# Performance work log

Hardware: AMD Instinct MI355X
Metric: run time of the kernel (lower is better)

Reference implementation:

```python
import jax, jax.numpy as jnp
import numpy as np

B, D, T = 16, 512, 2048
H = 2
HD = D // H

def setup_inputs() -> dict:
    key = jax.random.key(0)
    k1, k2, k3, k4 = jax.random.split(key, 4)
    s_in = 1.0 / np.sqrt(D)   # torch default-like uniform init for weight_matrix
    s_t = 1.0 / np.sqrt(T)    # nn.Linear default init bound
    xs = jax.random.normal(k1, (B, D, T), dtype=jnp.float32)
    W_KQ = jax.random.uniform(k2, (D, D), jnp.float32, -s_in, s_in)
    W_PV = jax.random.uniform(k3, (D, D), jnp.float32, -s_in, s_in)
    W_out = jax.random.uniform(k4, (T, T), jnp.float32, -s_t, s_t)
    return {"xs": xs, "W_KQ": W_KQ, "W_PV": W_PV, "W_out": W_out}

def reference(xs, W_KQ, W_PV, W_out):
    b, d, t = xs.shape
    xs_skip = xs[:, :, :-1]                                   # [B, D, T-1]
    # xskq = xs_skip^T @ W_KQ  -> [B, T-1, D]
    xskq = jnp.einsum('bds,dj->bsj', xs_skip, W_KQ)
    # split heads: [B, H, T-1, HD]
    xskq_split = xskq.reshape(b, t - 1, H, HD).transpose(0, 2, 1, 3)
    # xs reshaped to heads along feature dim: [B, H, HD, T]
    xs_r = xs.reshape(b, H, HD, t)
    attn_arg = jnp.matmul(xskq_split, xs_r)                   # [B, H, T-1, T], rho=1
    # NON-STANDARD: softmax over the head axis (size 2)
    sm = jax.nn.softmax(attn_arg, axis=1)
    # W_PV @ xs_skip -> [B, D, T-1], split into heads [B, H, HD, T-1]
    wpvx = jnp.einsum('id,bds->bis', W_PV, xs_skip).reshape(b, H, HD, t - 1)
    f_attn = jnp.matmul(wpvx, sm).reshape(b, d, t)            # [B, D, T]
    # output = Linear(T, T, bias=None) then take last token:
    # out[b, i] = sum_t f_attn[b, i, t] * W_out[T-1, t]
    out = jnp.einsum('bdt,t->bd', f_attn, W_out[-1])
    return out
```

## Files before the change

kernel.cpp:

```cpp
#include <hip/hip_runtime.h>
#include <hip/hip_bf16.h>

#define NB 16
#define ND 512
#define NT 2048
#define TM1 2047
#define NHD 256

typedef __attribute__((ext_vector_type(8))) short bf16x8;
typedef __attribute__((ext_vector_type(4))) float f32x4;
typedef unsigned short ushort_t;
typedef unsigned int uint_t;

#define G0_OFF    0ull
#define R0_OFF    32768ull
#define SX_OFF    40960ull
#define WSUM_OFF  49152ull
#define WKQT_OFF  49408ull
#define CHUNK_OFF 180480ull
#define BATCH_US  (2048ull * 512ull)
#define BATCH_FLOATS (2ull * 524288ull)

__device__ __forceinline__ ushort_t f2bf(float x) {
    union { float f; uint_t u; } v; v.f = x;
    uint_t r = v.u + 0x7FFFu + ((v.u >> 16) & 1u);
    return (ushort_t)(r >> 16);
}
__device__ __forceinline__ float bf2f(uint_t u) {
    union { uint_t u; float f; } v; v.u = u << 16;
    return v.f;
}

__device__ __forceinline__ void async_copy16(const ushort_t* g, ushort_t* l) {
    __builtin_amdgcn_global_load_lds(
        (const __attribute__((address_space(1))) void*)g,
        (__attribute__((address_space(3))) void*)l, 16, 0, 0);
}

#define FENCE() asm volatile("" ::: "memory")
#define BARRIER() do { FENCE(); __builtin_amdgcn_s_barrier(); FENCE(); } while (0)
#define WAITVM4() asm volatile("s_waitcnt vmcnt(4)" ::: "memory")
#define WAITVM0() asm volatile("s_waitcnt vmcnt(0)" ::: "memory")

__global__ __launch_bounds__(256) void k_cvt_xst(const float* __restrict__ xs,
                                                 ushort_t* __restrict__ xst, int b0,
                                                 const float* __restrict__ wkq,
                                                 ushort_t* __restrict__ wkqT,
                                                 const float* __restrict__ wlast,
                                                 float* __restrict__ wsum,
                                                 float* __restrict__ sxacc) {
    __shared__ float tile[64][257];
    __shared__ float sxl[64];
    const int t0 = blockIdx.x * 256, d0 = blockIdx.y * 64;
    const int cc = blockIdx.z;
    const float* xb = xs + (size_t)(b0 + cc) * ND * NT;
    ushort_t* xo = xst + (size_t)cc * BATCH_US;
    const int wave = threadIdx.x >> 6, lane = threadIdx.x & 63;
    if (threadIdx.x < 64) sxl[threadIdx.x] = 0.f;
    #pragma unroll
    for (int i = 0; i < 16; ++i) {
        const int row = wave * 16 + i;
        *(float4*)&tile[row][lane * 4] =
            *(const float4*)&xb[(size_t)(d0 + row) * NT + t0 + lane * 4];
    }
    __syncthreads();
    const int c8 = (threadIdx.x & 7) * 8;
    float sxp[8] = {0.f, 0.f, 0.f, 0.f, 0.f, 0.f, 0.f, 0.f};
    #pragma unroll
    for (int i = 0; i < 8; ++i) {
        const int t = i * 32 + (threadIdx.x >> 3);
        uint_t w[4];
        #pragma unroll
        for (int p = 0; p < 4; ++p)
            w[p] = (uint_t)f2bf(tile[c8 + 2 * p][t]) |
                   ((uint_t)f2bf(tile[c8 + 2 * p + 1][t]) << 16);
        *(uint4*)&xo[(size_t)(t0 + t) * ND + d0 + c8] = *(uint4*)w;
        if (t0 + t != 2047) {
            #pragma unroll
            for (int p = 0; p < 8; ++p) sxp[p] += tile[c8 + p][t];
        }
    }
    #pragma unroll
    for (int p = 0; p < 8; ++p) atomicAdd(&sxl[c8 + p], sxp[p]);
    __syncthreads();
    if (threadIdx.x < 64)
        atomicAdd(&sxacc[(size_t)(b0 + cc) * ND + d0 + threadIdx.x], sxl[threadIdx.x]);
    if (cc == 0 && b0 == 0) {
        __shared__ float ptile[32][33];
        const int bid = blockIdx.y * 8 + blockIdx.x;
        const int c = threadIdx.x & 31, r = threadIdx.x >> 5;
        #pragma unroll 1
        for (int q = 0; q < 4; ++q) {
            const int job = bid * 4 + q;
            const int j0 = (job & 15) * 32, dd0 = (job >> 4) * 32;
            __syncthreads();
            #pragma unroll
            for (int i = 0; i < 4; ++i)
                ptile[r + i * 8][c] = wkq[(size_t)(dd0 + r + i * 8) * ND + j0 + c];
            __syncthreads();
            #pragma unroll
            for (int i = 0; i < 4; ++i)
                wkqT[(size_t)(j0 + r + i * 8) * ND + dd0 + c] = f2bf(ptile[c][r + i * 8]);
        }
        if (bid == 0) {
            __shared__ float red[256];
            float s = 0.f;
            for (int t = threadIdx.x; t < NT; t += 256) s += wlast[t];
            red[threadIdx.x] = s;
            __syncthreads();
            for (int off = 128; off > 0; off >>= 1) {
                if (threadIdx.x < off) red[threadIdx.x] += red[threadIdx.x + off];
                __syncthreads();
            }
            if (threadIdx.x == 0) *wsum = red[0];
        }
    }
}

__device__ __forceinline__ void ld_frag4(bf16x8 (&dst)[4][2], const ushort_t* buf,
                                         int rbase, int l15, int quad, int swz) {
    #pragma unroll
    for (int i = 0; i < 4; ++i)
        #pragma unroll
        for (int kc = 0; kc < 2; ++kc)
            dst[i][kc] = *(const bf16x8*)&buf[(rbase + i * 16 + l15) * 64 + (((kc * 4 + quad) ^ swz) << 3)];
}
__device__ __forceinline__ void ld_frag2(bf16x8 (&dst)[2][2], const ushort_t* buf,
                                         int rbase, int l15, int quad, int swz) {
    #pragma unroll
    for (int i = 0; i < 2; ++i)
        #pragma unroll
        for (int kc = 0; kc < 2; ++kc)
            dst[i][kc] = *(const bf16x8*)&buf[(rbase + i * 16 + l15) * 64 + (((kc * 4 + quad) ^ swz) << 3)];
}
__device__ __forceinline__ void mfma8(f32x4 (&acc)[8][4], const bf16x8 (&a)[4][2],
                                      const bf16x8 (&bb)[2][2], int mbase, int nbase) {
    __builtin_amdgcn_s_setprio(1);
    #pragma unroll
    for (int kc = 0; kc < 2; ++kc)
        #pragma unroll
        for (int mi = 0; mi < 4; ++mi)
            #pragma unroll
            for (int nj = 0; nj < 2; ++nj)
                acc[mbase + mi][nbase + nj] = __builtin_amdgcn_mfma_f32_16x16x32_bf16(
                    a[mi][kc], bb[nj][kc], acc[mbase + mi][nbase + nj], 0, 0, 0);
    __builtin_amdgcn_s_setprio(0);
}

__device__ __forceinline__ void gemm8ph(const ushort_t* __restrict__ Ag,
                                        const ushort_t* __restrict__ Bg,
                                        ushort_t* __restrict__ smA0, ushort_t* __restrict__ smA1,
                                        ushort_t* __restrict__ smB0, ushort_t* __restrict__ smB1,
                                        f32x4 (&acc)[8][4]) {
    const int tid = threadIdx.x;
    const int wave = tid >> 6, lane = tid & 63;
    const int l15 = lane & 15, quad = lane >> 4;
    const int wm = wave >> 2;
    const int swz = l15 & 7;
    const int lrow = lane >> 3;
    const size_t lsrc = (size_t)lrow * ND + (size_t)(((lane & 7) ^ lrow) << 3);
    ushort_t* smA[2] = {smA0, smA1};
    ushort_t* smB[2] = {smB0, smB1};

#define STAGE(gb_, buf_, kt_, h_) do {                                        \
        const ushort_t* g_ = (gb_) + (size_t)((h_) * 128 + wave * 8) * ND +   \
                             (kt_) * 64 + lsrc;                               \
        ushort_t* l_ = (buf_) + (h_) * 8192 + wave * 512;                     \
        async_copy16(g_, l_);                                                 \
        async_copy16(g_ + (size_t)64 * ND, l_ + 4096);                        \
    } while (0)

    bf16x8 a[4][2], br[2][2][2];

    STAGE(Bg, smB[0], 0, 0); STAGE(Bg, smB[0], 0, 1);
    STAGE(Ag, smA[0], 0, 0); STAGE(Ag, smA[0], 0, 1);
    STAGE(Bg, smB[1], 1, 0); STAGE(Bg, smB[1], 1, 1);
    WAITVM4();
    BARRIER();

    #pragma unroll
    for (int j = 0; j < 4; ++j) {
        const int kO = 2 * j + 1;
        ld_frag4(a, smA[0], wm * 128, l15, quad, swz);
        ld_frag2(br[0], smB[0], (wave & 3) * 64, l15, quad, swz);
        STAGE(Ag, smA[1], kO, 0);
        BARRIER();
        mfma8(acc, a, br[0], 0, 0);
        BARRIER();
        ld_frag2(br[1], smB[0], (wave & 3) * 64 + 32, l15, quad, swz);
        STAGE(Ag, smA[1], kO, 1);
        BARRIER();
        mfma8(acc, a, br[1], 0, 2);
        BARRIER();
        ld_frag4(a, smA[0], wm * 128 + 64, l15, quad, swz);
        if (j < 3) STAGE(Bg, smB[0], 2 * j + 2, 0);
        BARRIER();
        mfma8(acc, a, br[0], 4, 0);
        BARRIER();
        if (j < 3) STAGE(Bg, smB[0], 2 * j + 2, 1);
        BARRIER();
        mfma8(acc, a, br[1], 4, 2);
        if (j < 3) { WAITVM4(); } else { WAITVM0(); }
        BARRIER();
        ld_frag4(a, smA[1], wm * 128, l15, quad, swz);
        ld_frag2(br[0], smB[1], (wave & 3) * 64, l15, quad, swz);
        if (j < 3) STAGE(Ag, smA[0], 2 * j + 2, 0);
        BARRIER();
        mfma8(acc, a, br[0], 0, 0);
        BARRIER();
        ld_frag2(br[1], smB[1], (wave & 3) * 64 + 32, l15, quad, swz);
        if (j < 3) STAGE(Ag, smA[0], 2 * j + 2, 1);
        BARRIER();
        mfma8(acc, a, br[1], 0, 2);
        BARRIER();
        ld_frag4(a, smA[1], wm * 128 + 64, l15, quad, swz);
        if (j < 3) STAGE(Bg, smB[1], kO + 2, 0);
        BARRIER();
        mfma8(acc, a, br[0], 4, 0);
        BARRIER();
        if (j < 3) STAGE(Bg, smB[1], kO + 2, 1);
        BARRIER();
        mfma8(acc, a, br[1], 4, 2);
        if (j < 3) WAITVM4();
        BARRIER();
    }
#undef STAGE
}

__global__ __launch_bounds__(512, 2) void k_qd(const ushort_t* __restrict__ xst,
                                               const ushort_t* __restrict__ wkqT,
                                               ushort_t* __restrict__ qdb) {
    __shared__ __align__(16) ushort_t smA[2][16384];
    __shared__ __align__(16) ushort_t smB[2][16384];
    const int lin = blockIdx.x + gridDim.x * (blockIdx.y + gridDim.y * blockIdx.z);
    const int nwg8 = (gridDim.x * gridDim.y * gridDim.z) >> 3;
    const int logical = (lin & 7) * nwg8 + (lin >> 3);
    const int jt = logical & 1;
    const int st = (logical >> 1) & 7;
    const int cc = logical >> 4;
    const int j0 = jt * 256, s0 = st * 256;

    const ushort_t* Ag = xst + (size_t)cc * BATCH_US + (size_t)s0 * ND;
    const ushort_t* Bg = wkqT + (size_t)j0 * ND;
    ushort_t* qo = qdb + (size_t)cc * BATCH_US;

    f32x4 acc[8][4];
    #pragma unroll
    for (int mi = 0; mi < 8; ++mi)
        #pragma unroll
        for (int nj = 0; nj < 4; ++nj) acc[mi][nj] = (f32x4){0.f, 0.f, 0.f, 0.f};

    gemm8ph(Ag, Bg, smA[0], smA[1], smB[0], smB[1], acc);

    const int tid = threadIdx.x;
    const int wave = tid >> 6, lane = tid & 63;
    const int l15 = lane & 15, quad = lane >> 4;
    const int wm = wave >> 2, wn = wave & 3;
    const float sgn = (j0 == 0) ? 1.f : -1.f;
    #pragma unroll
    for (int mi = 0; mi < 8; ++mi) {
        const int srow = s0 + wm * 128 + mi * 16 + quad * 4;
        #pragma unroll
        for (int nj = 0; nj < 4; ++nj) {
            const int jcol = j0 + wn * 64 + nj * 16 + l15;
            #pragma unroll
            for (int r = 0; r < 4; ++r)
                qo[(size_t)(srow + r) * ND + jcol] = f2bf(sgn * acc[mi][nj][r]);
        }
    }
}

__global__ __launch_bounds__(256, 4) void k_attn(const ushort_t* __restrict__ qdb,
                                                 const ushort_t* __restrict__ xst,
                                                 const float* __restrict__ wlast,
                                                 float* __restrict__ r0acc, int b0) {
    __shared__ __align__(16) ushort_t smA[8192];
    __shared__ __align__(16) ushort_t smB[8192];
    __shared__ float lds_g[128];
    const int lin = blockIdx.x + gridDim.x * (blockIdx.y + gridDim.y * blockIdx.z);
    const int nwg8 = (gridDim.x * gridDim.y * gridDim.z) >> 3;
    const int logical = (lin & 7) * nwg8 + (lin >> 3);
    const int st = logical & 15;
    const int tq = (logical >> 4) & 3;
    const int cc = logical >> 6;
    const int s0 = st * 128;
    const int b = b0 + cc;

    const int tid = threadIdx.x;
    const int wave = tid >> 6, lane = tid & 63;
    const int l15 = lane & 15, quad = lane >> 4;
    const int wm = wave >> 1, wn = wave & 1;
    const int swz = l15 & 7;
    const int lrow = lane >> 3;
    const size_t lsrc = (size_t)lrow * ND + (size_t)(((lane & 7) ^ lrow) << 3);
    const ushort_t* Ag = qdb + (size_t)cc * BATCH_US + (size_t)s0 * ND;
    const ushort_t* Bg = xst + (size_t)cc * BATCH_US + (size_t)(tq * 512) * ND;

#define STAGEA(kt_) do {                                                      \
        const size_t ko_ = (size_t)(kt_) * 64;                                \
        _Pragma("unroll")                                                     \
        for (int n_ = 0; n_ < 4; ++n_) {                                      \
            const int rb_ = wave * 32 + n_ * 8;                               \
            async_copy16(Ag + (size_t)rb_ * ND + ko_ + lsrc, smA + rb_ * 64); \
        }                                                                     \
    } while (0)
#define STAGEB(kt_, tt_) do {                                                 \
        const size_t ko_ = (size_t)(kt_) * 64;                                \
        const size_t ro_ = (size_t)(tt_) * 128;                               \
        _Pragma("unroll")                                                     \
        for (int n_ = 0; n_ < 4; ++n_) {                                      \
            const int rb_ = wave * 32 + n_ * 8;                               \
            async_copy16(Bg + (ro_ + rb_) * ND + ko_ + lsrc, smB + rb_ * 64); \
        }                                                                     \
    } while (0)
#define COMPUTE() do {                                                        \
        _Pragma("unroll")                                                     \
        for (int kc = 0; kc < 2; ++kc) {                                      \
            bf16x8 af_[4], bf_[4];                                            \
            _Pragma("unroll")                                                 \
            for (int mi = 0; mi < 4; ++mi)                                    \
                af_[mi] = *(const bf16x8*)&smA[(wm * 64 + mi * 16 + l15) * 64 \
                          + (((kc * 4 + quad) ^ swz) << 3)];                  \
            _Pragma("unroll")                                                 \
            for (int nj = 0; nj < 4; ++nj)                                    \
                bf_[nj] = *(const bf16x8*)&smB[(wn * 64 + nj * 16 + l15) * 64 \
                          + (((kc * 4 + quad) ^ swz) << 3)];                  \
            __builtin_amdgcn_s_setprio(1);                                    \
            _Pragma("unroll")                                                 \
            for (int mi = 0; mi < 4; ++mi)                                    \
                _Pragma("unroll")                                             \
                for (int nj = 0; nj < 4; ++nj)                                \
                    acc[mi][nj] = __builtin_amdgcn_mfma_f32_16x16x32_bf16(    \
                        af_[mi], bf_[nj], acc[mi][nj], 0, 0, 0);              \
            __builtin_amdgcn_s_setprio(0);                                    \
        }                                                                     \
    } while (0)

    f32x4 acc[4][4];
    float gp[4][4];
    #pragma unroll
    for (int mi = 0; mi < 4; ++mi)
        #pragma unroll
        for (int nj = 0; nj < 4; ++nj) { acc[mi][nj] = (f32x4){0.f, 0.f, 0.f, 0.f}; gp[mi][nj] = 0.f; }
    if (tid < 128) lds_g[tid] = 0.f;

    #pragma unroll 1
    for (int it = 0; it < 32; ++it) {
        const int kt = it & 7, tt = it >> 3;
        STAGEA(kt);
        STAGEB(kt, tt);
        WAITVM0();
        BARRIER();
        COMPUTE();
        if (kt == 7) {
            const int tb = tq * 512 + tt * 128;
            float wt[4];
            #pragma unroll
            for (int nj = 0; nj < 4; ++nj) wt[nj] = wlast[tb + wn * 64 + nj * 16 + l15];
            #pragma unroll
            for (int mi = 0; mi < 4; ++mi)
                #pragma unroll
                for (int r = 0; r < 4; ++r) {
                    #pragma unroll
                    for (int nj = 0; nj < 4; ++nj) {
                        const float e = __expf(-acc[mi][nj][r]);
                        gp[mi][r] = fmaf(__builtin_amdgcn_rcpf(1.f + e), wt[nj], gp[mi][r]);
                    }
                }
            #pragma unroll
            for (int mi = 0; mi < 4; ++mi)
                #pragma unroll
                for (int nj = 0; nj < 4; ++nj) acc[mi][nj] = (f32x4){0.f, 0.f, 0.f, 0.f};
        }
        BARRIER();
    }
#undef STAGEA
#undef STAGEB
#undef COMPUTE

    #pragma unroll
    for (int mi = 0; mi < 4; ++mi)
        #pragma unroll
        for (int r = 0; r < 4; ++r) {
            float v = gp[mi][r];
            v += __shfl_xor(v, 1);
            v += __shfl_xor(v, 2);
            v += __shfl_xor(v, 4);
            v += __shfl_xor(v, 8);
            if (l15 == 0) atomicAdd(&lds_g[wm * 64 + mi * 16 + quad * 4 + r], v);
        }
    __syncthreads();
    {
        const ushort_t* xrow = xst + (size_t)cc * BATCH_US + (size_t)s0 * ND;
        const int send = (st == 15) ? 127 : 128;
        float a0 = 0.f, a1 = 0.f;
        for (int si = 0; si < send; ++si) {
            const float gv = lds_g[si];
            const uint_t pk = *(const uint_t*)&xrow[(size_t)si * ND + tid * 2];
            a0 = fmaf(bf2f(pk & 0xFFFFu), gv, a0);
            a1 = fmaf(bf2f(pk >> 16), gv, a1);
        }
        atomicAdd(&r0acc[(size_t)b * ND + tid * 2], a0);
        atomicAdd(&r0acc[(size_t)b * ND + tid * 2 + 1], a1);
    }
}

__global__ __launch_bounds__(256) void k_out(const float* __restrict__ wpv,
                                             const float* __restrict__ r0acc,
                                             const float* __restrict__ sxacc,
                                             const float* __restrict__ wsum,
                                             float* __restrict__ out) {
    const int b = blockIdx.x;
    const int i0 = blockIdx.y * 256;
    __shared__ float rs[1024];
    const float wsv = *wsum;
    for (int i = threadIdx.x; i < ND; i += 256) {
        const float r0 = r0acc[b * ND + i];
        const float sx = sxacc[b * ND + i];
        rs[i] = r0;
        rs[ND + i] = fmaf(wsv, sx, -r0);
    }
    __syncthreads();
    const int i = i0 + threadIdx.x;
    const float* wrow = wpv + (size_t)i * ND;
    const float* rh = rs + (i >> 8) * ND;
    float acc = 0.f;
    for (int dd = 0; dd < ND; dd += 4) {
        const float4 wv = *(const float4*)(wrow + dd);
        acc += wv.x * rh[dd] + wv.y * rh[dd + 1] + wv.z * rh[dd + 2] + wv.w * rh[dd + 3];
    }
    out[b * ND + i] = acc;
}

extern "C" void kernel_launch(void* const* d_in, const int* in_sizes, int n_in,
                              void* d_out, int out_size, void* d_ws, size_t ws_size,
                              hipStream_t stream) {
    (void)in_sizes; (void)n_in; (void)out_size;
    const float* xs   = (const float*)d_in[0];
    const float* wkq  = (const float*)d_in[1];
    const float* wpv  = (const float*)d_in[2];
    const float* wout = (const float*)d_in[3];
    const float* wlast = wout + (size_t)(NT - 1) * NT;

    float* ws    = (float*)d_ws;
    float* r0acc = ws + R0_OFF;
    float* sxacc = ws + SX_OFF;
    float* wsum  = ws + WSUM_OFF;
    ushort_t* wkqT = (ushort_t*)(ws + WKQT_OFF);

    const size_t ws_floats = ws_size / 4;
    size_t avail = (ws_floats > CHUNK_OFF) ? (ws_floats - CHUNK_OFF) : 0;
    int C = (int)(avail / BATCH_FLOATS);
    if (C > NB) C = NB;
    if (C < 1) C = 1;
    ushort_t* qdb = (ushort_t*)(ws + CHUNK_OFF);
    ushort_t* xst = (ushort_t*)(ws + CHUNK_OFF + (size_t)C * 524288ull);

    hipMemsetAsync(r0acc, 0, 16384 * sizeof(float), stream);

    for (int b0 = 0; b0 < NB; b0 += C) {
        const int cb = (NB - b0 < C) ? (NB - b0) : C;
        k_cvt_xst<<<dim3(8, 8, cb), 256, 0, stream>>>(xs, xst, b0,
                                                      wkq, wkqT, wlast, wsum, sxacc);
        k_qd     <<<dim3(2, 8, cb),  512, 0, stream>>>(xst, wkqT, qdb);
        k_attn   <<<dim3(16, 4, cb), 256, 0, stream>>>(qdb, xst, wlast, r0acc, b0);
    }
    k_out<<<dim3(NB, 2), 256, 0, stream>>>(wpv, r0acc, sxacc, wsum, (float*)d_out);
}
```

Baseline: 263.0 us.

## Defer xs-weighted reduction from attention kernel to separate k_r kernel

```diff
diff --git a/kernel.cpp b/kernel.cpp
--- a/kernel.cpp
+++ b/kernel.cpp
@@ -273,7 +273,7 @@
 __global__ __launch_bounds__(256, 4) void k_attn(const ushort_t* __restrict__ qdb,
                                                  const ushort_t* __restrict__ xst,
                                                  const float* __restrict__ wlast,
-                                                 float* __restrict__ r0acc, int b0) {
+                                                 float* __restrict__ g0, int b0) {
     __shared__ __align__(16) ushort_t smA[8192];
     __shared__ __align__(16) ushort_t smB[8192];
     __shared__ float lds_g[128];
@@ -390,19 +390,32 @@
             if (l15 == 0) atomicAdd(&lds_g[wm * 64 + mi * 16 + quad * 4 + r], v);
         }
     __syncthreads();
-    {
-        const ushort_t* xrow = xst + (size_t)cc * BATCH_US + (size_t)s0 * ND;
-        const int send = (st == 15) ? 127 : 128;
-        float a0 = 0.f, a1 = 0.f;
-        for (int si = 0; si < send; ++si) {
-            const float gv = lds_g[si];
-            const uint_t pk = *(const uint_t*)&xrow[(size_t)si * ND + tid * 2];
-            a0 = fmaf(bf2f(pk & 0xFFFFu), gv, a0);
-            a1 = fmaf(bf2f(pk >> 16), gv, a1);
-        }
-        atomicAdd(&r0acc[(size_t)b * ND + tid * 2], a0);
-        atomicAdd(&r0acc[(size_t)b * ND + tid * 2 + 1], a1);
-    }
+    if (tid < 128) {
+        const int srow = s0 + tid;
+        if (srow < TM1) atomicAdd(&g0[b * TM1 + srow], lds_g[tid]);
+    }
+}
+
+__global__ __launch_bounds__(256) void k_r(const ushort_t* __restrict__ xst,
+                                           const float* __restrict__ g0,
+                                           float* __restrict__ r0acc, int b0) {
+    const int sc = blockIdx.x;
+    const int cc = blockIdx.y;
+    const int b = b0 + cc;
+    const ushort_t* xa = xst + (size_t)cc * BATCH_US;
+    const float* g = g0 + b * TM1;
+    const int d2 = threadIdx.x;
+    float a00 = 0.f, a01 = 0.f;
+    const int send = (sc == 31) ? 63 : 64;
+    for (int si = 0; si < send; ++si) {
+        const int s = sc * 64 + si;
+        const float gv = g[s];
+        const uint_t pk = *(const uint_t*)&xa[(size_t)s * ND + d2 * 2];
+        a00 = fmaf(bf2f(pk & 0xFFFFu), gv, a00);
+        a01 = fmaf(bf2f(pk >> 16), gv, a01);
+    }
+    atomicAdd(&r0acc[b * ND + d2 * 2], a00);
+    atomicAdd(&r0acc[b * ND + d2 * 2 + 1], a01);
 }
 
 __global__ __launch_bounds__(256) void k_out(const float* __restrict__ wpv,
@@ -443,6 +456,7 @@
     const float* wlast = wout + (size_t)(NT - 1) * NT;
 
     float* ws    = (float*)d_ws;
+    float* g0    = ws + G0_OFF;
     float* r0acc = ws + R0_OFF;
     float* sxacc = ws + SX_OFF;
     float* wsum  = ws + WSUM_OFF;
@@ -456,14 +470,15 @@
     ushort_t* qdb = (ushort_t*)(ws + CHUNK_OFF);
     ushort_t* xst = (ushort_t*)(ws + CHUNK_OFF + (size_t)C * 524288ull);
 
-    hipMemsetAsync(r0acc, 0, 16384 * sizeof(float), stream);
+    hipMemsetAsync(ws, 0, 49152 * sizeof(float), stream);
 
     for (int b0 = 0; b0 < NB; b0 += C) {
         const int cb = (NB - b0 < C) ? (NB - b0) : C;
         k_cvt_xst<<<dim3(8, 8, cb), 256, 0, stream>>>(xs, xst, b0,
                                                       wkq, wkqT, wlast, wsum, sxacc);
         k_qd     <<<dim3(2, 8, cb),  512, 0, stream>>>(xst, wkqT, qdb);
-        k_attn   <<<dim3(16, 4, cb), 256, 0, stream>>>(qdb, xst, wlast, r0acc, b0);
+        k_attn   <<<dim3(16, 4, cb), 256, 0, stream>>>(qdb, xst, wlast, g0, b0);
+        k_r      <<<dim3(32, cb),    256, 0, stream>>>(xst, g0, r0acc, b0);
     }
     k_out<<<dim3(NB, 2), 256, 0, stream>>>(wpv, r0acc, sxacc, wsum, (float*)d_out);
 }
```

Result: slower. 278.6 us (+6.0%).
